# Performance work log

Hardware: AMD Instinct MI355X
Metric: run time of the kernel (lower is better)

The kernel has to match this reference:

```python
import jax, jax.numpy as jnp
import numpy as np

N_ANT = 64      # n_antenna
K = 2           # branching factor
N_BEAM = 64     # n_narrow_beam
N_LAYER = 6     # log_K(N_BEAM); 5 Node layers + 1 Leaf layer
BATCH = 131072


def _dft_codebook():
    # Leaf DFT codebook: steering vectors at azimuths arccos(linspace(cos0, cos(pi-1e-6), N_BEAM))
    az = np.arccos(np.linspace(np.cos(0.0), np.cos(np.pi - 1e-6), N_BEAM))
    A = np.exp(1j * np.pi * np.outer(np.arange(N_ANT), np.cos(az))) / np.sqrt(N_ANT)
    return jnp.asarray(A, dtype=jnp.complex64)  # (N_ANT, N_BEAM)


def setup_inputs() -> dict:
    key = jax.random.key(0)
    keys = jax.random.split(key, N_LAYER)
    inp = {"xbatch": jax.random.normal(keys[0], (BATCH, 2 * N_ANT), dtype=jnp.float32)}
    for l in range(N_LAYER - 1):  # Node layers l=0..4, k^l nodes each, theta (nodes, N_ANT, K)
        inp[f"theta{l}"] = jax.random.normal(keys[l + 1], (K ** l, N_ANT, K), dtype=jnp.float32)
    return inp


def reference(xbatch, theta0, theta1, theta2, theta3, theta4):
    thetas = [theta0, theta1, theta2, theta3, theta4]
    B = xbatch.shape[0]
    # complex channel from stacked [real | imag] input
    h = jax.lax.complex(xbatch[:, :N_ANT], xbatch[:, N_ANT:])  # (B, N_ANT) complex64
    inv_scale = 1.0 / np.sqrt(N_ANT)

    # P holds path probabilities for all nodes at the current depth, flattened.
    P = jnp.ones((B, 1), dtype=xbatch.dtype)
    for theta in thetas:
        # PhaseShifter: W = exp(j*theta)/sqrt(N_ANT), per node  -> (n_nodes, N_ANT, K)
        W = jax.lax.complex(jnp.cos(theta), jnp.sin(theta)) * inv_scale
        y = jnp.einsum('ba,nak->bnk', h, W)          # (B, n_nodes, K) complex
        gain = y.real ** 2 + y.imag ** 2              # ComputePower
        p = jax.nn.softmax(gain, axis=-1)             # per-node softmax over K children
        P = (P[:, :, None] * p).reshape(B, -1)        # extend all tree paths by one layer

    # Leaf layer: fixed DFT codebook, softmax within each group of K narrow beams
    A = _dft_codebook()
    y = (h @ A).reshape(B, N_BEAM // K, K)            # (B, 32, 2) complex
    gain = y.real ** 2 + y.imag ** 2
    p = jax.nn.softmax(gain, axis=-1)
    P = (P[:, :, None] * p).reshape(B, N_BEAM)        # (B, N_BEAM) leaf path probabilities
    return P
```

## Files before the change

kernel.cpp:

```cpp
#include <hip/hip_runtime.h>
#include <math.h>

#define N_ANT 64
#define BATCH 131072
#define NSTEPS 63
#define TPB 1024
#define NBLK 512
#define EPR 32
#define ROUNDS 8
#define PSTR 130

typedef float f32x4 __attribute__((ext_vector_type(4)));
typedef float v2f   __attribute__((ext_vector_type(2)));
typedef _Float16 f16x8 __attribute__((ext_vector_type(8)));
typedef _Float16 f16x4 __attribute__((ext_vector_type(4)));

#define BAR_LGKM() asm volatile("s_waitcnt lgkmcnt(0)\n\ts_barrier" ::: "memory")

static __device__ __forceinline__ float fast_rcp(float x) {
#if __has_builtin(__builtin_amdgcn_rcpf)
    return __builtin_amdgcn_rcpf(x);
#else
    return 1.0f / x;
#endif
}

static __device__ __forceinline__ void dfs_next(int& l, int& n) {
    if (l < 5) { l = l + 1; n = 2 * n; }
    else {
        while (n & 1) { n >>= 1; l--; }
        n += 1;
    }
}

__global__ void fill_B(const float* __restrict__ t0, const float* __restrict__ t1,
                       const float* __restrict__ t2, const float* __restrict__ t3,
                       const float* __restrict__ t4,
                       _Float16* __restrict__ B1p) {
    const int t = blockIdx.x * 256 + threadIdx.x;
    const int L = t & 63;
    const int kstep = (t >> 6) & 3;
    const int ntile = t >> 8;
    const int n = ntile * 16 + (L & 15);
    const int kbase = kstep * 32 + (L >> 4) * 8;

    f16x8 h1 = {0,0,0,0,0,0,0,0};
    if (n < 252) {
        const int c = n >> 1, part = n & 1;
        const int s = c >> 1, kidx = c & 1;
        int l = 0, nn = 0;
        for (int i = 0; i < s; ++i) dfs_next(l, nn);

        const double step = (-2.0 + 5e-13) / 63.0;
        const double cosaz = 1.0 + (double)(2 * nn + kidx) * step;

#pragma unroll
        for (int j = 0; j < 8; ++j) {
            const int k = kbase + j;
            const int a = k & 63;
            const int hi = k >> 6;
            float wr, wi;
            if (l < 5) {
                const float* th = (l == 0) ? t0 : (l == 1) ? t1 : (l == 2) ? t2
                                 : (l == 3) ? t3 : t4;
                float theta = th[(nn * N_ANT + a) * 2 + kidx];
                float sn, cs;
                sincosf(theta, &sn, &cs);
                wr = cs * 0.125f; wi = sn * 0.125f;
            } else {
                double tph = (double)a * cosaz * 0.5;
                tph -= floor(tph);
                const float ang = (float)tph * 6.283185307179586f;
                float sn, cs;
                sincosf(ang, &sn, &cs);
                wr = cs * 0.125f;
                wi = sn * 0.125f;
            }
            float v = (part == 0) ? (hi == 0 ? wr : -wi)
                                  : (hi == 0 ? wi :  wr);
            h1[j] = (_Float16)v;
        }
    }
    *(f16x8*)(B1p + (size_t)t * 8) = h1;
}

__global__ __launch_bounds__(TPB) void beam_mfma(const float* __restrict__ x,
                                                 const _Float16* __restrict__ W1p,
                                                 float* __restrict__ out) {
    __shared__ _Float16 xb[2][4096];
    __shared__ float pb[2][EPR * PSTR];

    const int tid = threadIdx.x;
    const int w   = tid >> 6;
    const int L   = tid & 63;
    const int q   = L >> 4;
    const int e15 = L & 15;

    f16x8 w1f[4];
#pragma unroll
    for (int ks = 0; ks < 4; ++ks)
        w1f[ks] = *(const f16x8*)(W1p + (size_t)((w * 4 + ks) * 64 + L) * 8);

    int myl = -1, myn = 0;
    {
        int cl = 0, cn = 0;
        for (int s = 0; s < NSTEPS; ++s) {
            if (s == L) { myl = cl; myn = cn; }
            dfs_next(cl, cn);
        }
    }
    const int sd0 = (myn >> 4) & 1, sd1 = (myn >> 3) & 1, sd2 = (myn >> 2) & 1,
              sd3 = (myn >> 1) & 1, sd4 = myn & 1;
    const int a0 = 0;
    const int a1 = a0 + 1 + sd0 * 31;
    const int a2 = a1 + 1 + sd1 * 15;
    const int a3 = a2 + 1 + sd2 * 7;
    const int a4 = a3 + 1 + sd3 * 3;

    const int s_er = tid & 31;
    const int s_rt = tid >> 5;
    const int s_h  = s_rt & 1;
    const int s_q  = (s_rt >> 1) & 3;
    const int s_ks = s_rt >> 3;
    const int s_goff = s_er * 128 + s_ks * 32 + s_q * 8 + s_h * 4;
    const int s_loff = ((s_ks * 4 + s_q) * 32 + s_er) * 8 + s_h * 4;

    const long base = (long)blockIdx.x * (EPR * ROUNDS);

    auto tree_pass = [&](int bb, int rr) {
#pragma unroll
        for (int pass = 0; pass < 2; ++pass) {
            const int er = 2 * w + pass;
            const float* prow = &pb[bb][er * PSTR];
            if (myl == 5) {
                v2f own = *(const v2f*)(prow + 2 * L);
                v2f q0 = *(const v2f*)(prow + 2 * a0);
                v2f q1 = *(const v2f*)(prow + 2 * a1);
                v2f q2 = *(const v2f*)(prow + 2 * a2);
                v2f q3 = *(const v2f*)(prow + 2 * a3);
                v2f q4 = *(const v2f*)(prow + 2 * a4);
                float P = (sd0 ? q0.y : q0.x) * (sd1 ? q1.y : q1.x)
                        * (sd2 ? q2.y : q2.x) * (sd3 ? q3.y : q3.x)
                        * (sd4 ? q4.y : q4.x);
                *(v2f*)(out + (base + (long)rr * EPR + er) * 64 + 2 * myn) =
                    (v2f){P * own.x, P * own.y};
            }
        }
    };

    {
        float4 v = *(const float4*)(x + base * 128 + s_goff);
        f16x4 hv = {(_Float16)v.x, (_Float16)v.y, (_Float16)v.z, (_Float16)v.w};
        *(f16x4*)(&xb[0][s_loff]) = hv;
    }
    float4 nv = {0.f, 0.f, 0.f, 0.f};
    if (ROUNDS > 1) nv = *(const float4*)(x + (base + EPR) * 128 + s_goff);
    BAR_LGKM();

#pragma unroll 1
    for (int r = 0; r < ROUNDS; ++r) {
        const int cur = r & 1;
        float4 nv2 = {0.f, 0.f, 0.f, 0.f};
        if (r + 2 < ROUNDS)
            nv2 = *(const float4*)(x + (base + (long)(r + 2) * EPR) * 128 + s_goff);

        f32x4 acc0 = {0,0,0,0};
        f32x4 acc1 = {0,0,0,0};
#pragma unroll
        for (int ks = 0; ks < 4; ++ks) {
            const _Float16* xc = &xb[cur][(size_t)((ks * 4 + q) * 32) * 8];
            f16x8 b0 = *(const f16x8*)(xc + e15 * 8);
            f16x8 b1 = *(const f16x8*)(xc + (16 + e15) * 8);
            acc0 = __builtin_amdgcn_mfma_f32_16x16x32_f16(w1f[ks], b0, acc0, 0, 0, 0);
            acc1 = __builtin_amdgcn_mfma_f32_16x16x32_f16(w1f[ks], b1, acc1, 0, 0, 0);
        }

        if (r > 0) tree_pass(cur ^ 1, r - 1);

        const int u = 4 * w + q;
#pragma unroll
        for (int g = 0; g < 2; ++g) {
            f32x4 a = g ? acc1 : acc0;
            float g0 = fmaf(a.x, a.x, a.y * a.y);
            float g1 = fmaf(a.z, a.z, a.w * a.w);
            float m  = fmaxf(g0, g1);
            float e0 = __expf(g0 - m);
            float e1 = __expf(g1 - m);
            float inv = fast_rcp(e0 + e1);
            if (u < NSTEPS)
                *(v2f*)(&pb[cur][(g * 16 + e15) * PSTR + 2 * u]) =
                    (v2f){e0 * inv, e1 * inv};
        }

        if (r + 1 < ROUNDS) {
            f16x4 hv = {(_Float16)nv.x, (_Float16)nv.y, (_Float16)nv.z, (_Float16)nv.w};
            *(f16x4*)(&xb[cur ^ 1][s_loff]) = hv;
        }
        nv = nv2;

        BAR_LGKM();
    }

    tree_pass((ROUNDS - 1) & 1, ROUNDS - 1);
}

extern "C" void kernel_launch(void* const* d_in, const int* in_sizes, int n_in,
                              void* d_out, int out_size, void* d_ws, size_t ws_size,
                              hipStream_t stream) {
    const float* x  = (const float*)d_in[0];
    const float* t0 = (const float*)d_in[1];
    const float* t1 = (const float*)d_in[2];
    const float* t2 = (const float*)d_in[3];
    const float* t3 = (const float*)d_in[4];
    const float* t4 = (const float*)d_in[5];
    _Float16* W1p = (_Float16*)d_ws;

    fill_B<<<dim3(16), dim3(256), 0, stream>>>(t0, t1, t2, t3, t4, W1p);
    beam_mfma<<<dim3(NBLK), dim3(TPB), 0, stream>>>(x, W1p, (float*)d_out);
}
```

Before: 127.2 us.

## Double rows per round and store softmax probabilities in fp16 LDS

```diff
diff --git a/kernel.cpp b/kernel.cpp
--- a/kernel.cpp
+++ b/kernel.cpp
@@ -5,15 +5,15 @@
 #define BATCH 131072
 #define NSTEPS 63
 #define TPB 1024
-#define NBLK 512
-#define EPR 32
+#define NBLK 256
+#define EPR 64
 #define ROUNDS 8
-#define PSTR 130
+#define PSTRH 126
 
 typedef float f32x4 __attribute__((ext_vector_type(4)));
 typedef float v2f   __attribute__((ext_vector_type(2)));
 typedef _Float16 f16x8 __attribute__((ext_vector_type(8)));
-typedef _Float16 f16x4 __attribute__((ext_vector_type(4)));
+typedef _Float16 f16x2 __attribute__((ext_vector_type(2)));
 
 #define BAR_LGKM() asm volatile("s_waitcnt lgkmcnt(0)\n\ts_barrier" ::: "memory")
 
@@ -87,8 +87,8 @@
 __global__ __launch_bounds__(TPB) void beam_mfma(const float* __restrict__ x,
                                                  const _Float16* __restrict__ W1p,
                                                  float* __restrict__ out) {
-    __shared__ _Float16 xb[2][4096];
-    __shared__ float pb[2][EPR * PSTR];
+    __shared__ _Float16 xb[2][8192];
+    __shared__ _Float16 pb[2][EPR * PSTRH];
 
     const int tid = threadIdx.x;
     const int w   = tid >> 6;
@@ -117,70 +117,80 @@
     const int a3 = a2 + 1 + sd2 * 7;
     const int a4 = a3 + 1 + sd3 * 3;
 
-    const int s_er = tid & 31;
-    const int s_rt = tid >> 5;
-    const int s_h  = s_rt & 1;
-    const int s_q  = (s_rt >> 1) & 3;
-    const int s_ks = s_rt >> 3;
-    const int s_goff = s_er * 128 + s_ks * 32 + s_q * 8 + s_h * 4;
-    const int s_loff = ((s_ks * 4 + s_q) * 32 + s_er) * 8 + s_h * 4;
+    const int s_er = tid & 63;
+    const int s_rt = tid >> 6;
+    const int s_ks = s_rt >> 2;
+    const int s_q  = s_rt & 3;
+    const int s_goff = s_er * 128 + s_ks * 32 + s_q * 8;
+    const int s_loff = (s_rt * 64 + s_er) * 8;
 
     const long base = (long)blockIdx.x * (EPR * ROUNDS);
 
     auto tree_pass = [&](int bb, int rr) {
 #pragma unroll
-        for (int pass = 0; pass < 2; ++pass) {
-            const int er = 2 * w + pass;
-            const float* prow = &pb[bb][er * PSTR];
+        for (int pass = 0; pass < 4; ++pass) {
+            const int er = 4 * w + pass;
+            const _Float16* prow = &pb[bb][er * PSTRH];
             if (myl == 5) {
-                v2f own = *(const v2f*)(prow + 2 * L);
-                v2f q0 = *(const v2f*)(prow + 2 * a0);
-                v2f q1 = *(const v2f*)(prow + 2 * a1);
-                v2f q2 = *(const v2f*)(prow + 2 * a2);
-                v2f q3 = *(const v2f*)(prow + 2 * a3);
-                v2f q4 = *(const v2f*)(prow + 2 * a4);
-                float P = (sd0 ? q0.y : q0.x) * (sd1 ? q1.y : q1.x)
-                        * (sd2 ? q2.y : q2.x) * (sd3 ? q3.y : q3.x)
-                        * (sd4 ? q4.y : q4.x);
+                f16x2 ownh = *(const f16x2*)(prow + 2 * L);
+                f16x2 q0 = *(const f16x2*)(prow + 2 * a0);
+                f16x2 q1 = *(const f16x2*)(prow + 2 * a1);
+                f16x2 q2 = *(const f16x2*)(prow + 2 * a2);
+                f16x2 q3 = *(const f16x2*)(prow + 2 * a3);
+                f16x2 q4 = *(const f16x2*)(prow + 2 * a4);
+                float P = (float)(sd0 ? q0.y : q0.x) * (float)(sd1 ? q1.y : q1.x)
+                        * (float)(sd2 ? q2.y : q2.x) * (float)(sd3 ? q3.y : q3.x)
+                        * (float)(sd4 ? q4.y : q4.x);
                 *(v2f*)(out + (base + (long)rr * EPR + er) * 64 + 2 * myn) =
-                    (v2f){P * own.x, P * own.y};
+                    (v2f){P * (float)ownh.x, P * (float)ownh.y};
             }
         }
     };
 
     {
-        float4 v = *(const float4*)(x + base * 128 + s_goff);
-        f16x4 hv = {(_Float16)v.x, (_Float16)v.y, (_Float16)v.z, (_Float16)v.w};
-        *(f16x4*)(&xb[0][s_loff]) = hv;
-    }
-    float4 nv = {0.f, 0.f, 0.f, 0.f};
-    if (ROUNDS > 1) nv = *(const float4*)(x + (base + EPR) * 128 + s_goff);
+        float4 va = *(const float4*)(x + base * 128 + s_goff);
+        float4 vb = *(const float4*)(x + base * 128 + s_goff + 4);
+        f16x8 hv = {(_Float16)va.x, (_Float16)va.y, (_Float16)va.z, (_Float16)va.w,
+                    (_Float16)vb.x, (_Float16)vb.y, (_Float16)vb.z, (_Float16)vb.w};
+        *(f16x8*)(&xb[0][s_loff]) = hv;
+    }
+    float4 nva = {0.f,0.f,0.f,0.f}, nvb = {0.f,0.f,0.f,0.f};
+    if (ROUNDS > 1) {
+        nva = *(const float4*)(x + (base + EPR) * 128 + s_goff);
+        nvb = *(const float4*)(x + (base + EPR) * 128 + s_goff + 4);
+    }
     BAR_LGKM();
 
 #pragma unroll 1
     for (int r = 0; r < ROUNDS; ++r) {
         const int cur = r & 1;
-        float4 nv2 = {0.f, 0.f, 0.f, 0.f};
-        if (r + 2 < ROUNDS)
-            nv2 = *(const float4*)(x + (base + (long)(r + 2) * EPR) * 128 + s_goff);
-
-        f32x4 acc0 = {0,0,0,0};
-        f32x4 acc1 = {0,0,0,0};
+        float4 nv2a = {0.f,0.f,0.f,0.f}, nv2b = {0.f,0.f,0.f,0.f};
+        if (r + 2 < ROUNDS) {
+            nv2a = *(const float4*)(x + (base + (long)(r + 2) * EPR) * 128 + s_goff);
+            nv2b = *(const float4*)(x + (base + (long)(r + 2) * EPR) * 128 + s_goff + 4);
+        }
+
+        f32x4 acc0 = {0,0,0,0}, acc1 = {0,0,0,0};
+        f32x4 acc2 = {0,0,0,0}, acc3 = {0,0,0,0};
 #pragma unroll
         for (int ks = 0; ks < 4; ++ks) {
-            const _Float16* xc = &xb[cur][(size_t)((ks * 4 + q) * 32) * 8];
+            const _Float16* xc = &xb[cur][(size_t)((ks * 4 + q) * 64) * 8];
             f16x8 b0 = *(const f16x8*)(xc + e15 * 8);
             f16x8 b1 = *(const f16x8*)(xc + (16 + e15) * 8);
+            f16x8 b2 = *(const f16x8*)(xc + (32 + e15) * 8);
+            f16x8 b3 = *(const f16x8*)(xc + (48 + e15) * 8);
             acc0 = __builtin_amdgcn_mfma_f32_16x16x32_f16(w1f[ks], b0, acc0, 0, 0, 0);
             acc1 = __builtin_amdgcn_mfma_f32_16x16x32_f16(w1f[ks], b1, acc1, 0, 0, 0);
+            acc2 = __builtin_amdgcn_mfma_f32_16x16x32_f16(w1f[ks], b2, acc2, 0, 0, 0);
+            acc3 = __builtin_amdgcn_mfma_f32_16x16x32_f16(w1f[ks], b3, acc3, 0, 0, 0);
         }
 
         if (r > 0) tree_pass(cur ^ 1, r - 1);
 
         const int u = 4 * w + q;
 #pragma unroll
-        for (int g = 0; g < 2; ++g) {
-            f32x4 a = g ? acc1 : acc0;
+        for (int g = 0; g < 4; ++g) {
+            f32x4 a = (g == 0) ? acc0 : (g == 1) ? acc1 : (g == 2) ? acc2 : acc3;
             float g0 = fmaf(a.x, a.x, a.y * a.y);
             float g1 = fmaf(a.z, a.z, a.w * a.w);
             float m  = fmaxf(g0, g1);
@@ -188,15 +198,16 @@
             float e1 = __expf(g1 - m);
             float inv = fast_rcp(e0 + e1);
             if (u < NSTEPS)
-                *(v2f*)(&pb[cur][(g * 16 + e15) * PSTR + 2 * u]) =
-                    (v2f){e0 * inv, e1 * inv};
+                *(f16x2*)(&pb[cur][(g * 16 + e15) * PSTRH + 2 * u]) =
+                    (f16x2){(_Float16)(e0 * inv), (_Float16)(e1 * inv)};
         }
 
         if (r + 1 < ROUNDS) {
-            f16x4 hv = {(_Float16)nv.x, (_Float16)nv.y, (_Float16)nv.z, (_Float16)nv.w};
-            *(f16x4*)(&xb[cur ^ 1][s_loff]) = hv;
-        }
-        nv = nv2;
+            f16x8 hv = {(_Float16)nva.x, (_Float16)nva.y, (_Float16)nva.z, (_Float16)nva.w,
+                        (_Float16)nvb.x, (_Float16)nvb.y, (_Float16)nvb.z, (_Float16)nvb.w};
+            *(f16x8*)(&xb[cur ^ 1][s_loff]) = hv;
+        }
+        nva = nv2a; nvb = nv2b;
 
         BAR_LGKM();
     }
```

After: 127.1 us. No clear change (-0.1%).
